# Optimization experiments

Measured on AMD Instinct MI355X. Metric: run time of the kernel, lower is better.

Reference implementation:

```python
import jax, jax.numpy as jnp
import numpy as np

OBS_LEN = 20
PRED_LEN = 30
H = 64          # h_dim
E = 16          # embedding_dim
B = 32768       # num_agents
IN_FEAT = OBS_LEN * 2  # 40
EPS = 1e-5


def layer_norm(x, g, b):
    m = jnp.mean(x, axis=-1, keepdims=True)
    v = jnp.mean((x - m) ** 2, axis=-1, keepdims=True)
    return (x - m) / jnp.sqrt(v + EPS) * g + b


def setup_inputs() -> dict:
    key = jax.random.key(0)
    ks = jax.random.split(key, 16)
    s = 0.1
    return {
        "traj_abs": jax.random.normal(ks[0], (OBS_LEN, B, 2), jnp.float32),
        "traj_rel": jax.random.normal(ks[1], (OBS_LEN, B, 2), jnp.float32),
        "decoder_h": jax.random.normal(ks[2], (1, B, H), jnp.float32),
        # LSTM params (PyTorch gate order: i, f, g, o)
        "W_ih": jax.random.normal(ks[3], (4 * H, E), jnp.float32) * s,
        "W_hh": jax.random.normal(ks[4], (4 * H, H), jnp.float32) * s,
        "b_ih": jax.random.normal(ks[5], (4 * H,), jnp.float32) * s,
        "b_hh": jax.random.normal(ks[6], (4 * H,), jnp.float32) * s,
        # spatial_embedding: Linear(40 -> 16)
        "emb_W": jax.random.normal(ks[7], (E, IN_FEAT), jnp.float32) * s,
        "emb_b": jax.random.normal(ks[8], (E,), jnp.float32) * s,
        # hidden2pos: Linear(64 -> 2)
        "h2p_W": jax.random.normal(ks[9], (2, H), jnp.float32) * s,
        "h2p_b": jax.random.normal(ks[10], (2,), jnp.float32) * s,
        # LayerNorms
        "ln1_g": jnp.ones((IN_FEAT,), jnp.float32),
        "ln1_b": jnp.zeros((IN_FEAT,), jnp.float32),
        "ln2_g": jnp.ones((H,), jnp.float32),
        "ln2_b": jnp.zeros((H,), jnp.float32),
    }


def reference(traj_abs, traj_rel, decoder_h, W_ih, W_hh, b_ih, b_hh,
              emb_W, emb_b, h2p_W, h2p_b, ln1_g, ln1_b, ln2_g, ln2_b):
    # use_rel_disp=False branch; D=1, num_layers=1 => LSTM is a single cell.
    h0 = decoder_h[0]                      # (B, H)
    c0 = jnp.zeros_like(h0)

    def step(carry, _):
        traj, h, c = carry
        # faithful to torch .view(num_agents, -1): raw row-major reshape (20,B,2)->(B,40)
        x = jax.nn.leaky_relu(
            layer_norm(traj.reshape(B, IN_FEAT), ln1_g, ln1_b) @ emb_W.T + emb_b
        )  # (B, E)
        gates = x @ W_ih.T + b_ih + h @ W_hh.T + b_hh   # (B, 4H)
        i, f, g, o = jnp.split(gates, 4, axis=-1)
        c = jax.nn.sigmoid(f) * c + jax.nn.sigmoid(i) * jnp.tanh(g)
        h = jax.nn.sigmoid(o) * jnp.tanh(c)
        pos = layer_norm(h, ln2_g, ln2_b) @ h2p_W.T + h2p_b  # (B, 2)
        traj = jnp.concatenate([traj[1:], pos[None]], axis=0)  # roll -1 on dim 0, set last
        return (traj, h, c), pos

    _, pred = jax.lax.scan(step, (traj_abs, h0, c0), None, length=PRED_LEN)
    return pred  # (PRED_LEN, B, 2)
```

## Files before the change

kernel.cpp:

```cpp
#include <hip/hip_runtime.h>

#define NAGENTS 32768
#define SLAB    65536
#define SPLIT   1310720
#define SPLIT4  327680
#define PRED    30
#define IN_F    40
#define LN_EPS  1e-5f
#define APB     128
#define NBLK    (NAGENTS/APB)
#define BTH     1024
#define XSTRIDE 104
#define RSTR    72

typedef short bf16x8 __attribute__((ext_vector_type(8)));
typedef short bf16x4 __attribute__((ext_vector_type(4)));
typedef short bf16x2 __attribute__((ext_vector_type(2)));
typedef float f32x4  __attribute__((ext_vector_type(4)));

#define C_SGW  0
#define C_BW   16
#define C_G2   32
#define C_SG2  160
#define C_B2   162
#define C_BIAS 164
#define C_TOT  420

__device__ __forceinline__ float fsigmoid(float x){ return 1.f/(1.f+__expf(-x)); }
__device__ __forceinline__ float ftanh(float x){
    float t = __expf(-2.f*fabsf(x));
    float r = (1.f-t)/(1.f+t);
    return copysignf(r, x);
}
__device__ __forceinline__ float lrelu(float x){ return x > 0.f ? x : 0.01f*x; }
__device__ __forceinline__ short f2bf(float x){
    unsigned u = __float_as_uint(x);
    return (short)((u + 0x7FFFu + ((u>>16)&1u)) >> 16);
}
__device__ __forceinline__ float bf2f(short s){
    return __uint_as_float(((unsigned)(unsigned short)s) << 16);
}

__global__ __launch_bounds__(BTH, 4)
void persist_kernel(const float* __restrict__ traj,
                    float* __restrict__ out,
                    const float* __restrict__ dec_h,
                    const float* __restrict__ W_ih, const float* __restrict__ W_hh,
                    const float* __restrict__ b_ih, const float* __restrict__ b_hh,
                    const float* __restrict__ emb_W, const float* __restrict__ emb_b,
                    const float* __restrict__ h2p_W, const float* __restrict__ h2p_b,
                    const float* __restrict__ ln1_g, const float* __restrict__ ln1_b,
                    const float* __restrict__ ln2_g, const float* __restrict__ ln2_b,
                    int* __restrict__ flags)
{
    __shared__ short Rs[APB*RSTR];
    __shared__ short Xs[APB*XSTRIDE];
    __shared__ float Ds[APB*16];
    __shared__ float St[APB*2];
    __shared__ float cst[C_TOT];

    const int tid  = threadIdx.x;
    const int bid  = blockIdx.x;
    const int a0   = bid * APB;
    const int l    = tid & 63;
    const int wv   = tid >> 6;
    const int gang = wv >> 2;
    const int wvin = wv & 3;
    const int cl   = l & 15;
    const int kb   = l >> 4;
    const int nh   = wvin*16 + cl;

    if (tid < 16) {
        int e = tid;
        float s = 0.f, b = 0.f;
        for (int f = 0; f < IN_F; ++f) {
            float wf = emb_W[e*40 + f];
            s += ln1_g[f] * wf;
            b += ln1_b[f] * wf;
        }
        cst[C_SGW + e] = s;
        cst[C_BW + e]  = b + emb_b[e];
    }
    if (tid < 128) {
        int k = tid >> 1, d = tid & 1;
        cst[C_G2 + tid] = ln2_g[k] * h2p_W[d*64 + k];
    }
    if (tid < 2) {
        int d = tid;
        float s = 0.f, b = 0.f;
        for (int k = 0; k < 64; ++k) {
            float wf = h2p_W[d*64 + k];
            s += ln2_g[k] * wf;
            b += ln2_b[k] * wf;
        }
        cst[C_SG2 + d] = s;
        cst[C_B2 + d]  = b + h2p_b[d];
    }
    if (tid >= 256 && tid < 512) cst[C_BIAS + tid - 256] = b_ih[tid-256] + b_hh[tid-256];

    bf16x8 bw[4][3];
#pragma unroll
    for (int g = 0; g < 4; ++g)
#pragma unroll
        for (int ks = 0; ks < 3; ++ks) {
            int n = g*64 + nh;
            bf16x8 v;
#pragma unroll
            for (int j = 0; j < 8; ++j) {
                int k = ks*32 + kb*8 + j;
                float f = 0.f;
                if (k < 16)      f = W_ih[n*16 + k];
                else if (k < 80) f = W_hh[n*64 + (k-16)];
                v[j] = f2bf(f);
            }
            bw[g][ks] = v;
        }

    bf16x8 ew[2];
#pragma unroll
    for (int ks = 0; ks < 2; ++ks) {
        bf16x8 v;
#pragma unroll
        for (int j = 0; j < 8; ++j) {
            int k = ks*32 + kb*8 + j;
            float f = (k < IN_F) ? ln1_g[k] * emb_W[cl*40 + k] : 0.f;
            v[j] = f2bf(f);
        }
        ew[ks] = v;
    }

    for (int i = tid; i < APB*16; i += BTH) {
        int a = i >> 4, q = i & 15;
        float4 hv = ((const float4*)dec_h)[(a0 + a)*16 + q];
        bf16x4 hb;
        hb[0] = f2bf(hv.x); hb[1] = f2bf(hv.y);
        hb[2] = f2bf(hv.z); hb[3] = f2bf(hv.w);
        *(bf16x4*)&Xs[a*XSTRIDE + 16 + q*4] = hb;
    }
    if (tid < APB*2) {
        int a = tid >> 1, hf = tid & 1;
        *(bf16x8*)&Xs[a*XSTRIDE + 80 + hf*8] = bf16x8{0,0,0,0,0,0,0,0};
    }
    for (int i = tid; i < APB*3; i += BTH) {
        int a = i / 3, seg = i - a*3;
        *(bf16x8*)&Rs[a*RSTR + 40 + seg*8] = bf16x8{0,0,0,0,0,0,0,0};
    }

    float cs[2][4];
#pragma unroll
    for (int mt = 0; mt < 2; ++mt)
#pragma unroll
        for (int r = 0; r < 4; ++r) cs[mt][r] = 0.f;

    __syncthreads();

    for (int s = 0; s < PRED; ++s) {
        {
            const long Ob = (long)s*SLAB + (long)a0*IN_F - SPLIT;
            const long Oe = Ob + APB*IN_F;
            if (Oe > 0) {
                long o0 = Ob < 0 ? 0 : Ob;
                int i0 = (int)(o0 >> 8);
                int i1 = (int)((Oe - 1) >> 8);
                for (int i = i0 + tid; i <= i1; i += BTH) {
                    int t = i >> 8, p = i & 255;
                    while (__hip_atomic_load(&flags[p], __ATOMIC_ACQUIRE,
                                             __HIP_MEMORY_SCOPE_AGENT) < t + 1)
                        __builtin_amdgcn_s_sleep(1);
                }
            }
        }
        __syncthreads();

        {
            const int Gb4 = s*(SLAB/4) + bid*(APB*IN_F/4);
            for (int i = tid; i < APB*IN_F/4; i += BTH) {
                int a = i / 10, f4 = i - a*10;
                int G4 = Gb4 + i;
                float4 v = (G4 < SPLIT4) ? ((const float4*)traj)[G4]
                                         : ((const float4*)out)[G4 - SPLIT4];
                bf16x4 b;
                b[0] = f2bf(v.x); b[1] = f2bf(v.y);
                b[2] = f2bf(v.z); b[3] = f2bf(v.w);
                *(bf16x4*)&Rs[a*RSTR + f4*4] = b;
            }
        }
        __syncthreads();

        if (wv < 8) {
            f32x4 dacc = f32x4{0.f, 0.f, 0.f, 0.f};
            const short* base = &Rs[(wv*16 + cl)*RSTR + kb*8];
            bf16x8 a0f = *(const bf16x8*)(base);
            bf16x8 a1f = *(const bf16x8*)(base + 32);
            dacc = __builtin_amdgcn_mfma_f32_16x16x32_bf16(a0f, ew[0], dacc, 0, 0, 0);
            dacc = __builtin_amdgcn_mfma_f32_16x16x32_bf16(a1f, ew[1], dacc, 0, 0, 0);
#pragma unroll
            for (int r = 0; r < 4; ++r)
                Ds[(wv*16 + kb*4 + r)*16 + cl] = dacc[r];
        } else {
            int t2 = tid - 512;
            int a = t2 >> 2, p = t2 & 3;
            const bf16x8* rp = (const bf16x8*)&Rs[a*RSTR + p*16];
            bf16x8 v0 = rp[0], v1 = rp[1];
            float s1 = 0.f, s2 = 0.f;
#pragma unroll
            for (int j = 0; j < 8; ++j) {
                float f0 = bf2f(v0[j]), f1 = bf2f(v1[j]);
                s1 += f0 + f1; s2 += f0*f0 + f1*f1;
            }
            s1 += __shfl_xor(s1, 1, 64); s2 += __shfl_xor(s2, 1, 64);
            s1 += __shfl_xor(s1, 2, 64); s2 += __shfl_xor(s2, 2, 64);
            if (p == 0) {
                float m = s1 * (1.f/IN_F);
                St[a*2]   = m;
                St[a*2+1] = rsqrtf(s2*(1.f/IN_F) - m*m + LN_EPS);
            }
        }
        __syncthreads();

        {
            int a = tid >> 3, p = tid & 7, e0 = p*2;
            float m = St[a*2], inv = St[a*2+1];
            float D0 = Ds[a*16 + e0], D1 = Ds[a*16 + e0 + 1];
            float x0 = inv*(D0 - m*cst[C_SGW+e0  ]) + cst[C_BW+e0  ];
            float x1 = inv*(D1 - m*cst[C_SGW+e0+1]) + cst[C_BW+e0+1];
            bf16x2 xa;
            xa[0] = f2bf(lrelu(x0));
            xa[1] = f2bf(lrelu(x1));
            *(bf16x2*)&Xs[a*XSTRIDE + e0] = xa;
        }
        __syncthreads();

        f32x4 acc[2][4];
#pragma unroll
        for (int g = 0; g < 4; ++g) {
            float bb = cst[C_BIAS + g*64 + nh];
            acc[0][g] = f32x4{bb, bb, bb, bb};
            acc[1][g] = f32x4{bb, bb, bb, bb};
        }
#pragma unroll
        for (int mt = 0; mt < 2; ++mt) {
            const short* base = &Xs[(gang*32 + mt*16 + cl)*XSTRIDE + kb*8];
            bf16x8 af0 = *(const bf16x8*)(base);
            bf16x8 af1 = *(const bf16x8*)(base + 32);
            bf16x8 af2 = *(const bf16x8*)(base + 64);
#pragma unroll
            for (int g = 0; g < 4; ++g) {
                acc[mt][g] = __builtin_amdgcn_mfma_f32_16x16x32_bf16(af0, bw[g][0], acc[mt][g], 0, 0, 0);
                acc[mt][g] = __builtin_amdgcn_mfma_f32_16x16x32_bf16(af1, bw[g][1], acc[mt][g], 0, 0, 0);
                acc[mt][g] = __builtin_amdgcn_mfma_f32_16x16x32_bf16(af2, bw[g][2], acc[mt][g], 0, 0, 0);
            }
        }
        __syncthreads();

#pragma unroll
        for (int mt = 0; mt < 2; ++mt) {
            int abase = gang*32 + mt*16 + kb*4;
#pragma unroll
            for (int r = 0; r < 4; ++r) {
                float cn = fsigmoid(acc[mt][1][r]) * cs[mt][r]
                         + fsigmoid(acc[mt][0][r]) * ftanh(acc[mt][2][r]);
                float hn = fsigmoid(acc[mt][3][r]) * ftanh(cn);
                cs[mt][r] = cn;
                Xs[(abase + r)*XSTRIDE + 16 + nh] = f2bf(hn);
            }
        }
        __syncthreads();

        {
            int a = tid >> 3, p = tid & 7;
            bf16x8 hv = *(const bf16x8*)&Xs[a*XSTRIDE + 16 + p*8];
            float s1 = 0.f, s2 = 0.f, d0 = 0.f, d1 = 0.f;
#pragma unroll
            for (int j = 0; j < 8; ++j) {
                float f = bf2f(hv[j]);
                float2 gw = *(const float2*)&cst[C_G2 + (p*8 + j)*2];
                s1 += f; s2 += f*f;
                d0 += f*gw.x; d1 += f*gw.y;
            }
#pragma unroll
            for (int mk = 1; mk < 8; mk <<= 1) {
                s1 += __shfl_xor(s1, mk, 64);
                s2 += __shfl_xor(s2, mk, 64);
                d0 += __shfl_xor(d0, mk, 64);
                d1 += __shfl_xor(d1, mk, 64);
            }
            if (p < 2) {
                float m   = s1 * (1.f/64);
                float inv = rsqrtf(s2*(1.f/64) - m*m + LN_EPS);
                float dd  = (p == 0) ? d0 : d1;
                float val = inv*(dd - m*cst[C_SG2+p]) + cst[C_B2+p];
                __hip_atomic_store(&out[s*SLAB + (a0 + a)*2 + p], val,
                                   __ATOMIC_RELAXED, __HIP_MEMORY_SCOPE_AGENT);
            }
        }

        if (s != PRED-1) {
            __syncthreads();
            if (tid == 0)
                __hip_atomic_store(&flags[bid], s+1, __ATOMIC_RELAXED,
                                   __HIP_MEMORY_SCOPE_AGENT);
        }
    }
}

extern "C" void kernel_launch(void* const* d_in, const int* in_sizes, int n_in,
                              void* d_out, int out_size, void* d_ws, size_t ws_size,
                              hipStream_t stream) {
    const float* traj  = (const float*)d_in[0];
    const float* dec_h = (const float*)d_in[2];
    const float* W_ih  = (const float*)d_in[3];
    const float* W_hh  = (const float*)d_in[4];
    const float* b_ih  = (const float*)d_in[5];
    const float* b_hh  = (const float*)d_in[6];
    const float* emb_W = (const float*)d_in[7];
    const float* emb_b = (const float*)d_in[8];
    const float* h2p_W = (const float*)d_in[9];
    const float* h2p_b = (const float*)d_in[10];
    const float* ln1_g = (const float*)d_in[11];
    const float* ln1_b = (const float*)d_in[12];
    const float* ln2_g = (const float*)d_in[13];
    const float* ln2_b = (const float*)d_in[14];
    float* out = (float*)d_out;
    int*   flg = (int*)d_ws;

    persist_kernel<<<NBLK, BTH, 0, stream>>>(
        traj, out, dec_h, W_ih, W_hh, b_ih, b_hh, emb_W, emb_b,
        h2p_W, h2p_b, ln1_g, ln1_b, ln2_g, ln2_b, flg);
}
```

Before: 370.8 us.

## Merge flag wait into traj load, keep embedding result in registers, fast rcp

Measured after the change: 992.0 us. 2.68x slower.

```diff
diff --git a/kernel.cpp b/kernel.cpp
--- a/kernel.cpp
+++ b/kernel.cpp
@@ -1,4 +1,5 @@
 #include <hip/hip_runtime.h>
+#include <hip/hip_bf16.h>
 
 #define NAGENTS 32768
 #define SLAB    65536
@@ -15,21 +16,18 @@
 
 typedef short bf16x8 __attribute__((ext_vector_type(8)));
 typedef short bf16x4 __attribute__((ext_vector_type(4)));
-typedef short bf16x2 __attribute__((ext_vector_type(2)));
 typedef float f32x4  __attribute__((ext_vector_type(4)));
 
-#define C_SGW  0
-#define C_BW   16
-#define C_G2   32
-#define C_SG2  160
-#define C_B2   162
-#define C_BIAS 164
-#define C_TOT  420
-
-__device__ __forceinline__ float fsigmoid(float x){ return 1.f/(1.f+__expf(-x)); }
+#define C_G2   0
+#define C_SG2  128
+#define C_B2   130
+#define C_TOT  132
+
+__device__ __forceinline__ float frcp(float x){ return __builtin_amdgcn_rcpf(x); }
+__device__ __forceinline__ float fsigmoid(float x){ return frcp(1.f + __expf(-x)); }
 __device__ __forceinline__ float ftanh(float x){
     float t = __expf(-2.f*fabsf(x));
-    float r = (1.f-t)/(1.f+t);
+    float r = (1.f - t) * frcp(1.f + t);
     return copysignf(r, x);
 }
 __device__ __forceinline__ float lrelu(float x){ return x > 0.f ? x : 0.01f*x; }
@@ -39,6 +37,10 @@
 }
 __device__ __forceinline__ float bf2f(short s){
     return __uint_as_float(((unsigned)(unsigned short)s) << 16);
+}
+__device__ __forceinline__ unsigned pk_bf16(float a, float b){
+    __hip_bfloat162 h = __float22bfloat162_rn(float2{a, b});
+    return *reinterpret_cast<unsigned*>(&h);
 }
 
 __global__ __launch_bounds__(BTH, 4)
@@ -55,7 +57,6 @@
 {
     __shared__ short Rs[APB*RSTR];
     __shared__ short Xs[APB*XSTRIDE];
-    __shared__ float Ds[APB*16];
     __shared__ float St[APB*2];
     __shared__ float cst[C_TOT];
 
@@ -70,33 +71,30 @@
     const int kb   = l >> 4;
     const int nh   = wvin*16 + cl;
 
-    if (tid < 16) {
-        int e = tid;
-        float s = 0.f, b = 0.f;
-        for (int f = 0; f < IN_F; ++f) {
-            float wf = emb_W[e*40 + f];
-            s += ln1_g[f] * wf;
-            b += ln1_b[f] * wf;
-        }
-        cst[C_SGW + e] = s;
-        cst[C_BW + e]  = b + emb_b[e];
-    }
-    if (tid < 128) {
-        int k = tid >> 1, d = tid & 1;
-        cst[C_G2 + tid] = ln2_g[k] * h2p_W[d*64 + k];
-    }
+    if (tid < 128) cst[C_G2 + tid] = ln2_g[tid>>1] * h2p_W[(tid&1)*64 + (tid>>1)];
     if (tid < 2) {
         int d = tid;
-        float s = 0.f, b = 0.f;
+        float sg = 0.f, bb = 0.f;
         for (int k = 0; k < 64; ++k) {
             float wf = h2p_W[d*64 + k];
-            s += ln2_g[k] * wf;
-            b += ln2_b[k] * wf;
-        }
-        cst[C_SG2 + d] = s;
-        cst[C_B2 + d]  = b + h2p_b[d];
-    }
-    if (tid >= 256 && tid < 512) cst[C_BIAS + tid - 256] = b_ih[tid-256] + b_hh[tid-256];
+            sg += ln2_g[k] * wf;
+            bb += ln2_b[k] * wf;
+        }
+        cst[C_SG2 + d] = sg;
+        cst[C_B2 + d]  = bb + h2p_b[d];
+    }
+
+    float bb_r[4];
+#pragma unroll
+    for (int g = 0; g < 4; ++g) bb_r[g] = b_ih[g*64 + nh] + b_hh[g*64 + nh];
+
+    float sgw_c = 0.f, bw_c = 0.f;
+    for (int f = 0; f < IN_F; ++f) {
+        float wf = emb_W[cl*40 + f];
+        sgw_c += ln1_g[f] * wf;
+        bw_c  += ln1_b[f] * wf;
+    }
+    bw_c += emb_b[cl];
 
     bf16x8 bw[4][3];
 #pragma unroll
@@ -132,10 +130,8 @@
     for (int i = tid; i < APB*16; i += BTH) {
         int a = i >> 4, q = i & 15;
         float4 hv = ((const float4*)dec_h)[(a0 + a)*16 + q];
-        bf16x4 hb;
-        hb[0] = f2bf(hv.x); hb[1] = f2bf(hv.y);
-        hb[2] = f2bf(hv.z); hb[3] = f2bf(hv.w);
-        *(bf16x4*)&Xs[a*XSTRIDE + 16 + q*4] = hb;
+        uint2 pv{ pk_bf16(hv.x, hv.y), pk_bf16(hv.z, hv.w) };
+        *(uint2*)&Xs[a*XSTRIDE + 16 + q*4] = pv;
     }
     if (tid < APB*2) {
         int a = tid >> 1, hf = tid & 1;
@@ -155,48 +151,37 @@
     __syncthreads();
 
     for (int s = 0; s < PRED; ++s) {
-        {
-            const long Ob = (long)s*SLAB + (long)a0*IN_F - SPLIT;
-            const long Oe = Ob + APB*IN_F;
-            if (Oe > 0) {
-                long o0 = Ob < 0 ? 0 : Ob;
-                int i0 = (int)(o0 >> 8);
-                int i1 = (int)((Oe - 1) >> 8);
-                for (int i = i0 + tid; i <= i1; i += BTH) {
-                    int t = i >> 8, p = i & 255;
-                    while (__hip_atomic_load(&flags[p], __ATOMIC_ACQUIRE,
-                                             __HIP_MEMORY_SCOPE_AGENT) < t + 1)
-                        __builtin_amdgcn_s_sleep(1);
-                }
-            }
-        }
-        __syncthreads();
-
         {
             const int Gb4 = s*(SLAB/4) + bid*(APB*IN_F/4);
             for (int i = tid; i < APB*IN_F/4; i += BTH) {
                 int a = i / 10, f4 = i - a*10;
                 int G4 = Gb4 + i;
-                float4 v = (G4 < SPLIT4) ? ((const float4*)traj)[G4]
-                                         : ((const float4*)out)[G4 - SPLIT4];
-                bf16x4 b;
-                b[0] = f2bf(v.x); b[1] = f2bf(v.y);
-                b[2] = f2bf(v.z); b[3] = f2bf(v.w);
-                *(bf16x4*)&Rs[a*RSTR + f4*4] = b;
-            }
-        }
-        __syncthreads();
-
+                float4 v;
+                if (G4 < SPLIT4) {
+                    v = ((const float4*)traj)[G4];
+                } else {
+                    int of = G4 - SPLIT4;
+                    int t = of >> 14;
+                    int p = (of >> 6) & 255;
+                    while (__hip_atomic_load(&flags[p], __ATOMIC_ACQUIRE,
+                                             __HIP_MEMORY_SCOPE_AGENT) < t + 1)
+                        __builtin_amdgcn_s_sleep(1);
+                    v = ((const float4*)out)[of];
+                }
+                uint2 pv{ pk_bf16(v.x, v.y), pk_bf16(v.z, v.w) };
+                *(uint2*)&Rs[a*RSTR + f4*4] = pv;
+            }
+        }
+        __syncthreads();
+
+        f32x4 dacc;
         if (wv < 8) {
-            f32x4 dacc = f32x4{0.f, 0.f, 0.f, 0.f};
+            dacc = f32x4{0.f, 0.f, 0.f, 0.f};
             const short* base = &Rs[(wv*16 + cl)*RSTR + kb*8];
             bf16x8 a0f = *(const bf16x8*)(base);
             bf16x8 a1f = *(const bf16x8*)(base + 32);
             dacc = __builtin_amdgcn_mfma_f32_16x16x32_bf16(a0f, ew[0], dacc, 0, 0, 0);
             dacc = __builtin_amdgcn_mfma_f32_16x16x32_bf16(a1f, ew[1], dacc, 0, 0, 0);
-#pragma unroll
-            for (int r = 0; r < 4; ++r)
-                Ds[(wv*16 + kb*4 + r)*16 + cl] = dacc[r];
         } else {
             int t2 = tid - 512;
             int a = t2 >> 2, p = t2 & 3;
@@ -218,25 +203,22 @@
         }
         __syncthreads();
 
-        {
-            int a = tid >> 3, p = tid & 7, e0 = p*2;
-            float m = St[a*2], inv = St[a*2+1];
-            float D0 = Ds[a*16 + e0], D1 = Ds[a*16 + e0 + 1];
-            float x0 = inv*(D0 - m*cst[C_SGW+e0  ]) + cst[C_BW+e0  ];
-            float x1 = inv*(D1 - m*cst[C_SGW+e0+1]) + cst[C_BW+e0+1];
-            bf16x2 xa;
-            xa[0] = f2bf(lrelu(x0));
-            xa[1] = f2bf(lrelu(x1));
-            *(bf16x2*)&Xs[a*XSTRIDE + e0] = xa;
+        if (wv < 8) {
+#pragma unroll
+            for (int r = 0; r < 4; ++r) {
+                int a = wv*16 + kb*4 + r;
+                float m = St[a*2], inv = St[a*2+1];
+                float x = inv*(dacc[r] - m*sgw_c) + bw_c;
+                Xs[a*XSTRIDE + cl] = f2bf(lrelu(x));
+            }
         }
         __syncthreads();
 
         f32x4 acc[2][4];
 #pragma unroll
         for (int g = 0; g < 4; ++g) {
-            float bb = cst[C_BIAS + g*64 + nh];
-            acc[0][g] = f32x4{bb, bb, bb, bb};
-            acc[1][g] = f32x4{bb, bb, bb, bb};
+            acc[0][g] = f32x4{bb_r[g], bb_r[g], bb_r[g], bb_r[g]};
+            acc[1][g] = f32x4{bb_r[g], bb_r[g], bb_r[g], bb_r[g]};
         }
 #pragma unroll
         for (int mt = 0; mt < 2; ++mt) {
```
